# Optimization experiments

Measured on AMD Instinct MI355X. Metric: run time of the kernel, lower is better.

The kernel has to match this reference:

```python
import jax, jax.numpy as jnp
import numpy as np

N2 = 128      # time horizon (days)
M = 16384     # number of regions / batched chains
START = 6     # seeding window (days with externally seeded cases)


def setup_inputs() -> dict:
    key = jax.random.key(0)
    k0, k1, k2, k3, k4 = jax.random.split(key, 5)
    # reproduction numbers R_t in [0, 2)
    rt = jax.random.uniform(k0, (N2, M), dtype=jnp.float32) * 2.0
    deaths_gt = jax.random.uniform(k1, (N2, M), dtype=jnp.float32)
    # serial-interval distribution (positive, sums to 1 so the recurrence stays bounded)
    si_raw = jax.random.uniform(k2, (N2,), dtype=jnp.float32)
    SI = si_raw / jnp.sum(si_raw)
    f_raw = jax.random.uniform(k3, (N2, M), dtype=jnp.float32)
    f = f_raw / jnp.sum(f_raw, axis=0, keepdims=True) * 0.01
    # seeded cases for the first START days
    seed = jax.random.uniform(k4, (START, M), dtype=jnp.float32)
    return {"rt": rt, "deaths_gt": deaths_gt, "SI": SI, "f": f,
            "seed": seed, "start": START}


def _predict_cases(rt, SI, seed, start):
    # prediction[i, m] = rt[i, m] * sum_{j < i} prediction[j, m] * SI[i - j]
    # sequential triangular recurrence over time -> lax.scan with full carry.
    n2, m = rt.shape
    idx = jnp.arange(n2)
    pred0 = jnp.zeros((n2, m), rt.dtype).at[:start].set(seed)

    def step(pred, i):
        d = i - idx                                   # SI lag for each j
        w = jnp.where(d > 0, SI[jnp.clip(d, 0, n2 - 1)], 0.0)  # [N2], zero for j >= i
        conv = w @ pred                               # [M]
        row = jnp.where(i >= start, rt[i] * conv, pred[i])
        return pred.at[i].set(row), None

    pred, _ = jax.lax.scan(step, pred0, jnp.arange(n2))
    return pred


def _predict_deaths(pred, f, start):
    # E_deaths[i, m] = sum_{j <= i-2} pred[j, m] * f[i-j, m]
    # = causal per-region convolution with lags d = i-j >= 2 (so zero f[0], f[1]).
    n2, m = pred.shape
    f_eff = f.at[:2].set(0.0)
    conv = jax.vmap(lambda p, k: jnp.convolve(p, k)[:n2],
                    in_axes=1, out_axes=1)(pred, f_eff)   # [N2, M]
    i = jnp.arange(n2)[:, None]
    # rows before `start` are untouched by the loop (0), row 0 is set to 1e-9
    return jnp.where(i >= start, conv, jnp.where(i == 0, 1e-9, 0.0))


def reference(rt, deaths_gt, SI, f, seed, start):
    cases_pred = _predict_cases(rt, SI, seed, start)
    deaths_pred = _predict_deaths(cases_pred, f, start)
    return jnp.mean((deaths_pred - deaths_gt) ** 2)  # nn.MSELoss
```

## Files before the change

### kernel.cpp

```cpp
#include <hip/hip_runtime.h>

#define N2 128
#define MM 16384
#define START 6
#define CB 32
#define BT 256
#define PROWS 136
#define FROWS 152

__global__ __launch_bounds__(BT, 2) void npi_fused(
    const float* __restrict__ rt, const float* __restrict__ dgt,
    const float* __restrict__ si, const float* __restrict__ f,
    const float* __restrict__ seed, float* __restrict__ out)
{
    __shared__ float predT[PROWS * CB];
    __shared__ float fTd[FROWS * CB];
    __shared__ float part[4 * 16 * CB];
    __shared__ float si_s[N2];
    __shared__ float lred[4];

    const int t = threadIdx.x;
    const int c = t & (CB - 1);
    const int w = t >> 6;
    const int g = t >> 5;
    const int hw = g & 1;
    const int m = blockIdx.x * CB + c;

    float fregs[16];
#pragma unroll
    for (int q = 0; q < 16; ++q)
        fregs[q] = f[((g << 4) + q) * MM + m];

    if (t < N2) si_s[t] = si[t];
    if (g < START) predT[(g << 5) + c] = seed[g * MM + m];
    predT[((128 + g) << 5) + c] = 0.f;
    fTd[(g << 5) + c] = 0.f;
    fTd[((8 + g) << 5) + c] = 0.f;
    if (g < 2) fTd[((16 + g) << 5) + c] = 0.f;
    fTd[((144 + g) << 5) + c] = 0.f;

    float r16v[16];
#pragma unroll
    for (int k = 0; k < 16; ++k)
        r16v[k] = rt[k * MM + m];

    __syncthreads();

    float sr[16];
#pragma unroll
    for (int k = 1; k < 16; ++k) sr[k] = si_s[k];

    {
        float v[16];
#pragma unroll
        for (int k = 0; k < 16; ++k) {
            if (k < START) {
                v[k] = predT[(k << 5) + c];
            } else {
                float s = 0.f;
#pragma unroll
                for (int kk = 0; kk < 16; ++kk)
                    if (kk < k) s += v[kk] * sr[k - kk];
                v[k] = r16v[k] * s;
            }
        }
        if (w == 3 && hw == 0) {
#pragma unroll
            for (int k = START; k < 16; ++k) predT[(k << 5) + c] = v[k];
        }
    }
    __syncthreads();

    for (int b = 1; b < 8; ++b) {
        const int i0 = b << 4;
        const int nst = b << 1;
#pragma unroll
        for (int k = 0; k < 16; ++k)
            r16v[k] = rt[(i0 + k) * MM + m];

        const int jhi = nst * (g + 1);
        const int base = i0 - jhi + 1;
        float c16[16];
#pragma unroll
        for (int e = 0; e < 16; ++e) c16[e] = si_s[base + e];
        float acc[16];
#pragma unroll
        for (int k = 0; k < 16; ++k) acc[k] = 0.f;
#pragma unroll
        for (int u = 0; u < 14; ++u) {
            if (u < nst) {
                float p = predT[((jhi - 1 - u) << 5) + c];
#pragma unroll
                for (int k = 0; k < 16; ++k)
                    acc[k] += p * c16[(u + k) & 15];
                if (u + 1 < nst) c16[u] = si_s[base + 16 + u];
            }
        }
#pragma unroll
        for (int k = 0; k < 16; ++k)
            acc[k] += __shfl_xor(acc[k], 32, 64);
        if (hw == 0) {
#pragma unroll
            for (int k = 0; k < 16; ++k)
                part[(((w << 4) + k) << 5) + c] = acc[k];
        }
        __syncthreads();

        float v[16];
#pragma unroll
        for (int k = 0; k < 16; ++k) {
            float s = part[(k << 5) + c] + part[((16 + k) << 5) + c]
                    + part[((32 + k) << 5) + c] + part[((48 + k) << 5) + c];
#pragma unroll
            for (int kk = 0; kk < 16; ++kk)
                if (kk < k) s += v[kk] * sr[k - kk];
            v[k] = r16v[k] * s;
        }
        {
            float a0, a1;
            if (w == 0)      { a0 = hw ? v[2]  : v[0];  a1 = hw ? v[3]  : v[1];  }
            else if (w == 1) { a0 = hw ? v[6]  : v[4];  a1 = hw ? v[7]  : v[5];  }
            else if (w == 2) { a0 = hw ? v[10] : v[8];  a1 = hw ? v[11] : v[9];  }
            else             { a0 = hw ? v[14] : v[12]; a1 = hw ? v[15] : v[13]; }
            const int r0 = i0 + (w << 2) + (hw << 1);
            predT[(r0 << 5) + c] = a0;
            predT[((r0 + 1) << 5) + c] = a1;
        }
        __syncthreads();
    }

#pragma unroll
    for (int q = 0; q < 16; ++q) {
        int d = (g << 4) + q;
        fTd[((16 + d) << 5) + c] = (d < 2) ? 0.f : fregs[q];
    }
    __syncthreads();

    float lsum = 0.f;
    if (hw == 0) {
        float dv = dgt[w * MM + m];
        float e0 = (w == 0) ? (1e-9f - dv) : dv;
        lsum += e0 * e0;
        if (w < 2) {
            float d2 = dgt[(4 + w) * MM + m];
            lsum += d2 * d2;
        }
    }

#pragma unroll
    for (int half = 0; half < 2; ++half) {
        const int n = half ? (7 - w) : w;
        const int i0 = START + (n << 4);
        const int jhi2 = i0 + 14;
        const int steps = jhi2 >> 1;
        const int jh = hw ? jhi2 : (jhi2 >> 1);
        const int fb = 17 + i0 - jh;

        float dg[16];
#pragma unroll
        for (int k = 0; k < 16; ++k)
            dg[k] = (i0 + k < N2) ? dgt[(i0 + k) * MM + m] : 0.f;

        float cf[16];
#pragma unroll
        for (int e = 0; e < 16; ++e) cf[e] = fTd[((fb + e) << 5) + c];
        float acc[16];
#pragma unroll
        for (int k = 0; k < 16; ++k) acc[k] = 0.f;

        for (int sb = 0; sb < steps; sb += 16) {
#pragma unroll
            for (int u = 0; u < 16; ++u) {
                int s = sb + u;
                if (s < steps) {
                    float p = predT[((jh - 1 - s) << 5) + c];
#pragma unroll
                    for (int k = 0; k < 16; ++k)
                        acc[k] += p * cf[(u + k) & 15];
                    cf[u] = fTd[((fb + 16 + s) << 5) + c];
                }
            }
        }
#pragma unroll
        for (int k = 0; k < 16; ++k)
            acc[k] += __shfl_xor(acc[k], 32, 64);
        if (hw == 0) {
#pragma unroll
            for (int k = 0; k < 16; ++k) {
                if (i0 + k < N2) {
                    float diff = acc[k] - dg[k];
                    lsum += diff * diff;
                }
            }
        }
    }

#pragma unroll
    for (int off = 32; off > 0; off >>= 1)
        lsum += __shfl_down(lsum, off, 64);
    if ((t & 63) == 0) lred[w] = lsum;
    __syncthreads();
    if (t == 0)
        atomicAdd(out, (lred[0] + lred[1] + lred[2] + lred[3]) *
                       (1.0f / ((float)N2 * (float)MM)));
}

extern "C" void kernel_launch(void* const* d_in, const int* in_sizes, int n_in,
                              void* d_out, int out_size, void* d_ws, size_t ws_size,
                              hipStream_t stream) {
    const float* rt   = (const float*)d_in[0];
    const float* dgt  = (const float*)d_in[1];
    const float* si   = (const float*)d_in[2];
    const float* f    = (const float*)d_in[3];
    const float* seed = (const float*)d_in[4];

    hipMemsetAsync(d_out, 0, sizeof(float), stream);
    npi_fused<<<dim3(MM / CB), dim3(BT), 0, stream>>>(
        rt, dgt, si, f, seed, (float*)d_out);
}
```

Before: 105.9 us.

## Double block size to 512 threads and repartition recurrence and death convolution work

Raises the block from 256 to 512 threads (8 waves), giving each half-wave a smaller slice of the history sum and of the deaths convolution (8 output rows instead of 16). The per-block triangular solve is now done by wave 0 only, after a two-stage shared-memory reduction through a new hrow buffer, and rt rows are prefetched one block ahead. The aim is more parallelism and fewer registers per thread, at the cost of an extra barrier per time block and leaving most waves idle during the serial solve.

```diff
diff --git a/kernel.cpp b/kernel.cpp
--- a/kernel.cpp
+++ b/kernel.cpp
@@ -4,20 +4,21 @@
 #define MM 16384
 #define START 6
 #define CB 32
-#define BT 256
+#define BT 512
 #define PROWS 136
 #define FROWS 152
 
-__global__ __launch_bounds__(BT, 2) void npi_fused(
+__global__ __launch_bounds__(BT, 4) void npi_fused(
     const float* __restrict__ rt, const float* __restrict__ dgt,
     const float* __restrict__ si, const float* __restrict__ f,
     const float* __restrict__ seed, float* __restrict__ out)
 {
     __shared__ float predT[PROWS * CB];
     __shared__ float fTd[FROWS * CB];
-    __shared__ float part[4 * 16 * CB];
+    __shared__ float part[8 * 16 * CB];
+    __shared__ float hrow[16 * CB];
     __shared__ float si_s[N2];
-    __shared__ float lred[4];
+    __shared__ float lred[8];
 
     const int t = threadIdx.x;
     const int c = t & (CB - 1);
@@ -26,31 +27,30 @@
     const int hw = g & 1;
     const int m = blockIdx.x * CB + c;
 
-    float fregs[16];
-#pragma unroll
-    for (int q = 0; q < 16; ++q)
-        fregs[q] = f[((g << 4) + q) * MM + m];
+    float fregs[8];
+#pragma unroll
+    for (int q = 0; q < 8; ++q)
+        fregs[q] = f[((g << 3) + q) * MM + m];
 
     if (t < N2) si_s[t] = si[t];
     if (g < START) predT[(g << 5) + c] = seed[g * MM + m];
-    predT[((128 + g) << 5) + c] = 0.f;
+    if (g < 8) predT[((128 + g) << 5) + c] = 0.f;
     fTd[(g << 5) + c] = 0.f;
-    fTd[((8 + g) << 5) + c] = 0.f;
     if (g < 2) fTd[((16 + g) << 5) + c] = 0.f;
-    fTd[((144 + g) << 5) + c] = 0.f;
+    if (g < 8) fTd[((144 + g) << 5) + c] = 0.f;
 
     float r16v[16];
-#pragma unroll
-    for (int k = 0; k < 16; ++k)
-        r16v[k] = rt[k * MM + m];
-
+    if (w == 0) {
+#pragma unroll
+        for (int k = 0; k < 16; ++k) r16v[k] = rt[k * MM + m];
+    }
     __syncthreads();
 
     float sr[16];
 #pragma unroll
     for (int k = 1; k < 16; ++k) sr[k] = si_s[k];
 
-    {
+    if (w == 0) {
         float v[16];
 #pragma unroll
         for (int k = 0; k < 16; ++k) {
@@ -64,21 +64,18 @@
                 v[k] = r16v[k] * s;
             }
         }
-        if (w == 3 && hw == 0) {
-#pragma unroll
-            for (int k = START; k < 16; ++k) predT[(k << 5) + c] = v[k];
-        }
+#pragma unroll
+        for (int k = START; k < 16; ++k)
+            if (hw == 0) predT[(k << 5) + c] = v[k];
+#pragma unroll
+        for (int k = 0; k < 16; ++k)
+            r16v[k] = rt[(16 + k) * MM + m];
     }
     __syncthreads();
 
     for (int b = 1; b < 8; ++b) {
         const int i0 = b << 4;
-        const int nst = b << 1;
-#pragma unroll
-        for (int k = 0; k < 16; ++k)
-            r16v[k] = rt[(i0 + k) * MM + m];
-
-        const int jhi = nst * (g + 1);
+        const int jhi = b * (g + 1);
         const int base = i0 - jhi + 1;
         float c16[16];
 #pragma unroll
@@ -87,13 +84,13 @@
 #pragma unroll
         for (int k = 0; k < 16; ++k) acc[k] = 0.f;
 #pragma unroll
-        for (int u = 0; u < 14; ++u) {
-            if (u < nst) {
+        for (int u = 0; u < 7; ++u) {
+            if (u < b) {
                 float p = predT[((jhi - 1 - u) << 5) + c];
 #pragma unroll
                 for (int k = 0; k < 16; ++k)
                     acc[k] += p * c16[(u + k) & 15];
-                if (u + 1 < nst) c16[u] = si_s[base + 16 + u];
+                if (u + 1 < b) c16[u & 15] = si_s[base + 16 + u];
             }
         }
 #pragma unroll
@@ -106,89 +103,91 @@
         }
         __syncthreads();
 
-        float v[16];
-#pragma unroll
-        for (int k = 0; k < 16; ++k) {
-            float s = part[(k << 5) + c] + part[((16 + k) << 5) + c]
-                    + part[((32 + k) << 5) + c] + part[((48 + k) << 5) + c];
-#pragma unroll
-            for (int kk = 0; kk < 16; ++kk)
-                if (kk < k) s += v[kk] * sr[k - kk];
-            v[k] = r16v[k] * s;
-        }
         {
-            float a0, a1;
-            if (w == 0)      { a0 = hw ? v[2]  : v[0];  a1 = hw ? v[3]  : v[1];  }
-            else if (w == 1) { a0 = hw ? v[6]  : v[4];  a1 = hw ? v[7]  : v[5];  }
-            else if (w == 2) { a0 = hw ? v[10] : v[8];  a1 = hw ? v[11] : v[9];  }
-            else             { a0 = hw ? v[14] : v[12]; a1 = hw ? v[15] : v[13]; }
-            const int r0 = i0 + (w << 2) + (hw << 1);
-            predT[(r0 << 5) + c] = a0;
-            predT[((r0 + 1) << 5) + c] = a1;
+            float s = 0.f;
+#pragma unroll
+            for (int ww = 0; ww < 8; ++ww)
+                s += part[(((ww << 4) + g) << 5) + c];
+            hrow[(g << 5) + c] = s;
         }
         __syncthreads();
-    }
-
-#pragma unroll
-    for (int q = 0; q < 16; ++q) {
-        int d = (g << 4) + q;
+
+        if (w == 0) {
+            float v[16];
+#pragma unroll
+            for (int k = 0; k < 16; ++k) {
+                float s = hrow[(k << 5) + c];
+#pragma unroll
+                for (int kk = 0; kk < 16; ++kk)
+                    if (kk < k) s += v[kk] * sr[k - kk];
+                v[k] = r16v[k] * s;
+            }
+#pragma unroll
+            for (int k = 0; k < 8; ++k) {
+                float val = hw ? v[8 + k] : v[k];
+                int row = i0 + (hw << 3) + k;
+                predT[(row << 5) + c] = val;
+            }
+            if (b < 7) {
+#pragma unroll
+                for (int k = 0; k < 16; ++k)
+                    r16v[k] = rt[(i0 + 16 + k) * MM + m];
+            }
+        }
+        __syncthreads();
+    }
+
+#pragma unroll
+    for (int q = 0; q < 8; ++q) {
+        int d = (g << 3) + q;
         fTd[((16 + d) << 5) + c] = (d < 2) ? 0.f : fregs[q];
     }
     __syncthreads();
 
     float lsum = 0.f;
-    if (hw == 0) {
-        float dv = dgt[w * MM + m];
-        float e0 = (w == 0) ? (1e-9f - dv) : dv;
-        lsum += e0 * e0;
-        if (w < 2) {
-            float d2 = dgt[(4 + w) * MM + m];
-            lsum += d2 * d2;
-        }
-    }
-
-#pragma unroll
-    for (int half = 0; half < 2; ++half) {
-        const int n = half ? (7 - w) : w;
-        const int i0 = START + (n << 4);
-        const int jhi2 = i0 + 14;
-        const int steps = jhi2 >> 1;
-        const int jh = hw ? jhi2 : (jhi2 >> 1);
+    if (g >= 10) {
+        int i = g - 10;
+        float dv = dgt[i * MM + m];
+        float e0 = (i == 0) ? (1e-9f - dv) : dv;
+        lsum = e0 * e0;
+    }
+
+#pragma unroll
+    for (int pass = 0; pass < 2; ++pass) {
+        const int n = pass ? (15 - w) : w;
+        const int i0 = START + (n << 3);
+        const int jhi = i0 + 6;
+        const int steps = jhi >> 1;
+        const int jh = hw ? jhi : steps;
         const int fb = 17 + i0 - jh;
-
-        float dg[16];
-#pragma unroll
-        for (int k = 0; k < 16; ++k)
-            dg[k] = (i0 + k < N2) ? dgt[(i0 + k) * MM + m] : 0.f;
-
-        float cf[16];
-#pragma unroll
-        for (int e = 0; e < 16; ++e) cf[e] = fTd[((fb + e) << 5) + c];
-        float acc[16];
-#pragma unroll
-        for (int k = 0; k < 16; ++k) acc[k] = 0.f;
-
-        for (int sb = 0; sb < steps; sb += 16) {
-#pragma unroll
-            for (int u = 0; u < 16; ++u) {
+        float cf[8];
+#pragma unroll
+        for (int e = 0; e < 8; ++e) cf[e] = fTd[((fb + e) << 5) + c];
+        float acc8[8];
+#pragma unroll
+        for (int k = 0; k < 8; ++k) acc8[k] = 0.f;
+        for (int sb = 0; sb < steps; sb += 8) {
+#pragma unroll
+            for (int u = 0; u < 8; ++u) {
                 int s = sb + u;
                 if (s < steps) {
                     float p = predT[((jh - 1 - s) << 5) + c];
 #pragma unroll
-                    for (int k = 0; k < 16; ++k)
-                        acc[k] += p * cf[(u + k) & 15];
-                    cf[u] = fTd[((fb + 16 + s) << 5) + c];
+                    for (int k = 0; k < 8; ++k)
+                        acc8[k] += p * cf[(u + k) & 7];
+                    cf[u] = fTd[((fb + 8 + s) << 5) + c];
                 }
             }
         }
 #pragma unroll
-        for (int k = 0; k < 16; ++k)
-            acc[k] += __shfl_xor(acc[k], 32, 64);
-        if (hw == 0) {
-#pragma unroll
-            for (int k = 0; k < 16; ++k) {
-                if (i0 + k < N2) {
-                    float diff = acc[k] - dg[k];
+        for (int k = 0; k < 8; ++k)
+            acc8[k] += __shfl_xor(acc8[k], 32, 64);
+        if (hw == pass) {
+#pragma unroll
+            for (int k = 0; k < 8; ++k) {
+                int i = i0 + k;
+                if (i < N2) {
+                    float diff = acc8[k] - dgt[i * MM + m];
                     lsum += diff * diff;
                 }
             }
@@ -200,9 +199,12 @@
         lsum += __shfl_down(lsum, off, 64);
     if ((t & 63) == 0) lred[w] = lsum;
     __syncthreads();
-    if (t == 0)
-        atomicAdd(out, (lred[0] + lred[1] + lred[2] + lred[3]) *
-                       (1.0f / ((float)N2 * (float)MM)));
+    if (t == 0) {
+        float tot = 0.f;
+#pragma unroll
+        for (int ww = 0; ww < 8; ++ww) tot += lred[ww];
+        atomicAdd(out, tot * (1.0f / ((float)N2 * (float)MM)));
+    }
 }
 
 extern "C" void kernel_launch(void* const* d_in, const int* in_sizes, int n_in,
```

Result: slower. 110.8 us (+4.7%).

## Alias shared buffers, raise occupancy bound, restructure intra-block recurrence

Applied to the files above, without the earlier changes.

Overlaps the partial-sum buffer and the death-kernel buffer in one shared array, shrinks the padded prediction rows, and raises the launch-bounds occupancy hint from 2 to 4 blocks per CU. The fTd zero padding moves to after the recurrence phase so it does not collide with the aliased partial-sum buffer. The in-block 16-step triangular recurrence changes from pulling over all previous values to pushing each new value forward into accumulators, which shortens the dependency chain on the critical path. The tighter register budget from the occupancy hint may cause spills given the many 16-element register arrays.

```diff
diff --git a/kernel.cpp b/kernel.cpp
--- a/kernel.cpp
+++ b/kernel.cpp
@@ -5,19 +5,20 @@
 #define START 6
 #define CB 32
 #define BT 256
-#define PROWS 136
+#define PROWS 132
 #define FROWS 152
 
-__global__ __launch_bounds__(BT, 2) void npi_fused(
+__global__ __launch_bounds__(BT, 4) void npi_fused(
     const float* __restrict__ rt, const float* __restrict__ dgt,
     const float* __restrict__ si, const float* __restrict__ f,
     const float* __restrict__ seed, float* __restrict__ out)
 {
     __shared__ float predT[PROWS * CB];
-    __shared__ float fTd[FROWS * CB];
-    __shared__ float part[4 * 16 * CB];
+    __shared__ float funion[FROWS * CB];
     __shared__ float si_s[N2];
     __shared__ float lred[4];
+    float* part = funion;
+    float* fTd  = funion;
 
     const int t = threadIdx.x;
     const int c = t & (CB - 1);
@@ -33,11 +34,7 @@
 
     if (t < N2) si_s[t] = si[t];
     if (g < START) predT[(g << 5) + c] = seed[g * MM + m];
-    predT[((128 + g) << 5) + c] = 0.f;
-    fTd[(g << 5) + c] = 0.f;
-    fTd[((8 + g) << 5) + c] = 0.f;
-    if (g < 2) fTd[((16 + g) << 5) + c] = 0.f;
-    fTd[((144 + g) << 5) + c] = 0.f;
+    if (g < 4) predT[((128 + g) << 5) + c] = 0.f;
 
     float r16v[16];
 #pragma unroll
@@ -51,18 +48,18 @@
     for (int k = 1; k < 16; ++k) sr[k] = si_s[k];
 
     {
-        float v[16];
+        float p_[16], v[16];
+#pragma unroll
+        for (int k = 0; k < 16; ++k) p_[k] = 0.f;
 #pragma unroll
         for (int k = 0; k < 16; ++k) {
-            if (k < START) {
-                v[k] = predT[(k << 5) + c];
-            } else {
-                float s = 0.f;
-#pragma unroll
-                for (int kk = 0; kk < 16; ++kk)
-                    if (kk < k) s += v[kk] * sr[k - kk];
-                v[k] = r16v[k] * s;
-            }
+            float vk;
+            if (k < START) vk = predT[(k << 5) + c];
+            else vk = r16v[k] * (p_[k] + sr[1] * v[k - 1]);
+            v[k] = vk;
+#pragma unroll
+            for (int k2 = k + 2; k2 < 16; ++k2)
+                p_[k2] += sr[k2 - k] * vk;
         }
         if (w == 3 && hw == 0) {
 #pragma unroll
@@ -93,7 +90,7 @@
 #pragma unroll
                 for (int k = 0; k < 16; ++k)
                     acc[k] += p * c16[(u + k) & 15];
-                if (u + 1 < nst) c16[u] = si_s[base + 16 + u];
+                if (u + 1 < nst) c16[u & 15] = si_s[base + 16 + u];
             }
         }
 #pragma unroll
@@ -106,15 +103,19 @@
         }
         __syncthreads();
 
-        float v[16];
+        float p_[16], v[16];
+#pragma unroll
+        for (int k = 0; k < 16; ++k)
+            p_[k] = part[(k << 5) + c] + part[((16 + k) << 5) + c]
+                  + part[((32 + k) << 5) + c] + part[((48 + k) << 5) + c];
 #pragma unroll
         for (int k = 0; k < 16; ++k) {
-            float s = part[(k << 5) + c] + part[((16 + k) << 5) + c]
-                    + part[((32 + k) << 5) + c] + part[((48 + k) << 5) + c];
-#pragma unroll
-            for (int kk = 0; kk < 16; ++kk)
-                if (kk < k) s += v[kk] * sr[k - kk];
-            v[k] = r16v[k] * s;
+            float vk = (k == 0) ? (r16v[0] * p_[0])
+                                : (r16v[k] * (p_[k] + sr[1] * v[k - 1]));
+            v[k] = vk;
+#pragma unroll
+            for (int k2 = k + 2; k2 < 16; ++k2)
+                p_[k2] += sr[k2 - k] * vk;
         }
         {
             float a0, a1;
@@ -134,6 +135,9 @@
         int d = (g << 4) + q;
         fTd[((16 + d) << 5) + c] = (d < 2) ? 0.f : fregs[q];
     }
+    fTd[((g << 1) << 5) + c] = 0.f;
+    fTd[(((g << 1) + 1) << 5) + c] = 0.f;
+    fTd[((144 + g) << 5) + c] = 0.f;
     __syncthreads();
 
     float lsum = 0.f;
@@ -148,8 +152,8 @@
     }
 
 #pragma unroll
-    for (int half = 0; half < 2; ++half) {
-        const int n = half ? (7 - w) : w;
+    for (int pass = 0; pass < 2; ++pass) {
+        const int n = pass ? (7 - w) : w;
         const int i0 = START + (n << 4);
         const int jhi2 = i0 + 14;
         const int steps = jhi2 >> 1;
```

Result: no change. 107.1 us (+1.1%).
